# Kernel optimization log

Measured on AMD Instinct MI355X. Metric: run time of the kernel, lower is better.

The kernel has to match this reference:

```python
import jax, jax.numpy as jnp
import numpy as np

SEQ_LEN = 512
D_MODEL = 512
N_HEADS = 8
KERNEL = 7
E_DIM = D_MODEL // N_HEADS  # d_values = 64
PAD = KERNEL // 2


def _gen_D(L):
    D = np.zeros((L - 1, L), dtype=np.float32)
    D[:, 1:] += np.eye(L - 1, dtype=np.float32)
    D[:, :-1] -= np.eye(L - 1, dtype=np.float32)
    return D


def setup_inputs() -> dict:
    key = jax.random.key(0)
    k1, k2, k3 = jax.random.split(key, 3)
    B = 16
    values = jax.random.normal(k1, (B, SEQ_LEN, N_HEADS, E_DIM), dtype=jnp.float32)
    # second-order difference operator, then SVD of D^T D (as in __init__)
    D = _gen_D(SEQ_LEN - 1) @ _gen_D(SEQ_LEN)          # (L-2, L)
    U_np, S_np, _ = np.linalg.svd(D.T @ D)             # (L, L), (L,)
    U = jnp.asarray(U_np, dtype=jnp.float32)
    S = jnp.asarray(S_np, dtype=jnp.float32)
    # Conv1d(E, 1, kernel) parameters
    bound = 1.0 / np.sqrt(E_DIM * KERNEL)
    conv_w = jax.random.uniform(k2, (1, E_DIM, KERNEL), minval=-bound, maxval=bound, dtype=jnp.float32)
    conv_b = jax.random.uniform(k3, (1,), minval=-bound, maxval=bound, dtype=jnp.float32)
    return {"values": values, "conv_w": conv_w, "conv_b": conv_b, "U": U, "S": S}


def reference(values, conv_w, conv_b, U, S):
    B, L, H, E = values.shape
    # lambda predictor: conv1d over length with replicate padding, then 1+elu
    x = values.transpose(0, 2, 3, 1).reshape(B * H, E, L)          # (BH, E, L)
    xp = jnp.pad(x, ((0, 0), (0, 0), (PAD, PAD)), mode='edge')
    y = jax.lax.conv_general_dilated(
        xp, conv_w, window_strides=(1,), padding='VALID',
        dimension_numbers=('NCH', 'OIH', 'NCH'))                   # (BH, 1, L)
    y = y + conv_b[None, :, None]
    lambdas = 1.0 + jax.nn.elu(y).reshape(B, H, L).transpose(0, 2, 1)  # (B, L, H)
    # diagonal reweighting in the U basis: U diag(1/(1+lambda*S)) U^T @ values
    inv = 1.0 / (1.0 + jnp.einsum('blh,l->bhl', lambdas, S))       # (B, H, L)
    t = jnp.einsum('jm,bjhd->bhmd', U, values)                      # project onto U columns
    t = t * inv[..., None]                                          # diagonal scale (fused, no LxL diag)
    out = jnp.einsum('im,bhmd->bihd', U, t)                         # (B, L, H, E)
    return out
```

## Files before the change

### kernel.cpp

```cpp
#include <hip/hip_runtime.h>
#include <hip/hip_bf16.h>
#include <cstdint>
#include <cmath>

#define LSEQ 512
#define EDIM 64
#define NBIG 8192

typedef __attribute__((ext_vector_type(8))) short short8;
typedef __attribute__((ext_vector_type(8))) unsigned short ushort8v;
typedef __attribute__((ext_vector_type(4))) float f32x4;

__device__ __forceinline__ unsigned short f2bf(float f) {
    union { float f; unsigned int u; } x; x.f = f;
    unsigned int r = x.u + 0x7FFFu + ((x.u >> 16) & 1u);
    return (unsigned short)(r >> 16);
}

__device__ __forceinline__ void async_copy16(void* lds, const void* g) {
    auto g1 = (const __attribute__((address_space(1))) void*)g;
    auto l3 = (__attribute__((address_space(3))) void*)lds;
    __builtin_amdgcn_global_load_lds(g1, l3, 16, 0, 0);
}

__device__ __forceinline__ void store16_swz(unsigned short* rowptr, int cbase,
                                            int q, int row,
                                            const unsigned short* o) {
    int x = row & 7, x1 = x >> 1, x0 = x & 1;
    unsigned short* dst = rowptr + cbase + ((q ^ x1) << 4);
    ushort8v lo = *(const ushort8v*)o;
    ushort8v hi = *(const ushort8v*)(o + 8);
    if (x0) { *(ushort8v*)dst = hi; *(ushort8v*)(dst + 8) = lo; }
    else    { *(ushort8v*)dst = lo; *(ushort8v*)(dst + 8) = hi; }
}

__global__ __launch_bounds__(256) void prep_kernel(
        const float* __restrict__ vals, const float* __restrict__ U,
        const float* __restrict__ cw, const float* __restrict__ cb,
        const float* __restrict__ S,
        unsigned short* __restrict__ Vpp, unsigned short* __restrict__ Ut,
        unsigned short* __restrict__ Ub, float* __restrict__ inv) {
    __shared__ float Ls[70 * 65];
    __shared__ float red[16][64];
    __shared__ float wcoef[448];
    int id = blockIdx.x;
    int t = threadIdx.x;

    if (id < 1024) {
        int b = id >> 6, h = (id >> 3) & 7, jt = id & 7;
        int j0 = jt * 64;
        for (int idx = t; idx < 448; idx += 256) wcoef[idx] = cw[idx];
        const float* base = vals + (size_t)b * 262144 + h * 64;
        #pragma unroll
        for (int i = 0; i < 5; ++i) {
            int idx = i * 256 + t;
            if (idx < 1120) {
                int row = idx >> 4, c4 = (idx & 15) * 4;
                int grow = j0 + row - 3;
                grow = grow < 0 ? 0 : (grow > 511 ? 511 : grow);
                float4 v = *(const float4*)(base + (size_t)grow * 512 + c4);
                float* d = &Ls[row * 65 + c4];
                d[0] = v.x; d[1] = v.y; d[2] = v.z; d[3] = v.w;
            }
        }
        __syncthreads();

        {
            int e = t & 63, q = t >> 6;
            unsigned short o[16];
            #pragma unroll
            for (int jj = 0; jj < 16; ++jj)
                o[jj] = f2bf(Ls[(3 + q * 16 + jj) * 65 + e]);
            int n = b * 512 + h * 64 + e;
            store16_swz(Vpp + (size_t)n * 512, j0, q, n, o);
        }

        {
            int lg = t & 15, q16 = t >> 4;
            int l0 = lg * 4, e0 = q16 * 4;
            float rv[10][4];
            #pragma unroll
            for (int r = 0; r < 10; ++r)
                #pragma unroll
                for (int je = 0; je < 4; ++je)
                    rv[r][je] = Ls[(l0 + r) * 65 + e0 + je];
            float a4[4] = {0.f, 0.f, 0.f, 0.f};
            #pragma unroll
            for (int kk = 0; kk < 7; ++kk) {
                #pragma unroll
                for (int je = 0; je < 4; ++je) {
                    float w = wcoef[(e0 + je) * 7 + kk];
                    #pragma unroll
                    for (int dl = 0; dl < 4; ++dl)
                        a4[dl] += rv[dl + kk][je] * w;
                }
            }
            #pragma unroll
            for (int dl = 0; dl < 4; ++dl) red[q16][l0 + dl] = a4[dl];
        }
        __syncthreads();
        if (t < 64) {
            float y = cb[0];
            #pragma unroll
            for (int g = 0; g < 16; ++g) y += red[g][t];
            float lam = (y > 0.f) ? (1.f + y) : expf(y);
            inv[(size_t)(b * 8 + h) * 512 + j0 + t] = 1.f / (1.f + lam * S[j0 + t]);
        }
    } else {
        int id2 = id - 1024;
        int j0 = (id2 >> 3) * 64, m0 = (id2 & 7) * 64;
        int r = t >> 2, q = t & 3;
        int c16 = q * 16;
        float v[16];
        const float* src = U + (size_t)(j0 + r) * 512 + m0 + c16;
        #pragma unroll
        for (int k = 0; k < 16; k += 4) {
            float4 vv = *(const float4*)(src + k);
            v[k] = vv.x; v[k+1] = vv.y; v[k+2] = vv.z; v[k+3] = vv.w;
        }
        {
            unsigned short o[16];
            #pragma unroll
            for (int k = 0; k < 16; ++k) o[k] = f2bf(v[k]);
            store16_swz(Ub + (size_t)(j0 + r) * 512, m0, q, j0 + r, o);
        }
        #pragma unroll
        for (int k = 0; k < 16; ++k) Ls[r * 65 + c16 + k] = v[k];
        __syncthreads();
        {
            unsigned short o[16];
            #pragma unroll
            for (int k = 0; k < 16; ++k) o[k] = f2bf(Ls[(c16 + k) * 65 + r]);
            store16_swz(Ut + (size_t)(m0 + r) * 512, j0, q, m0 + r, o);
        }
    }
}

template<int EPI>
__launch_bounds__(256, 1)
__global__ void gemm_kernel(const unsigned short* __restrict__ A,
                            const unsigned short* __restrict__ B,
                            const float* __restrict__ inv,
                            unsigned short* __restrict__ Tout,
                            float* __restrict__ Out) {
    __shared__ __align__(16) unsigned short As[2][128 * 64];
    __shared__ __align__(16) unsigned short Bs[2][128 * 64];

    int bid = blockIdx.x;
    bid = (bid & 7) * 32 + (bid >> 3);
    int mt = bid & 3, nt = bid >> 2;
    int m0 = mt * 128, n0 = nt * 128;
    int t = threadIdx.x, lane = t & 63, wave = t >> 6;
    int wm = wave >> 1, wn = wave & 1;
    int l15 = lane & 15, l4 = lane >> 4;

    f32x4 acc[4][4] = {};

    const unsigned short* Ab = A + (size_t)(m0 + (t >> 3)) * 512 + (t & 7) * 8;
    const unsigned short* Bb = B + (size_t)(n0 + (t >> 3)) * 512 + (t & 7) * 8;

    auto STAGE = [&](int buf, int kk) {
        int ko = kk * 64;
        unsigned short* ap = &As[buf][t * 8];
        unsigned short* bp = &Bs[buf][t * 8];
        #pragma unroll
        for (int c = 0; c < 4; ++c) {
            async_copy16(ap + c * 2048, Ab + (size_t)(32 * c) * 512 + ko);
            async_copy16(bp + c * 2048, Bb + (size_t)(32 * c) * 512 + ko);
        }
    };
    auto COMPUTE = [&](int buf) {
        #pragma unroll
        for (int k2 = 0; k2 < 2; ++k2) {
            short8 a[4], bf[4];
            #pragma unroll
            for (int i = 0; i < 4; ++i) {
                int row = wm * 64 + i * 16 + l15;
                a[i] = *(const short8*)&As[buf][row * 64 + (((k2 * 4 + l4) ^ (row & 7)) << 3)];
            }
            #pragma unroll
            for (int j = 0; j < 4; ++j) {
                int row = wn * 64 + j * 16 + l15;
                bf[j] = *(const short8*)&Bs[buf][row * 64 + (((k2 * 4 + l4) ^ (row & 7)) << 3)];
            }
            #pragma unroll
            for (int i = 0; i < 4; ++i)
                #pragma unroll
                for (int j = 0; j < 4; ++j)
                    acc[i][j] = __builtin_amdgcn_mfma_f32_16x16x32_bf16(a[i], bf[j], acc[i][j], 0, 0, 0);
        }
    };

    STAGE(0, 0);
    __syncthreads();
    int cur = 0;
    #pragma unroll
    for (int kk = 0; kk < 7; ++kk) {
        STAGE(cur ^ 1, kk + 1);
        COMPUTE(cur);
        __syncthreads();
        cur ^= 1;
    }
    COMPUTE(cur);

    #pragma unroll
    for (int i = 0; i < 4; ++i) {
        int mb = m0 + wm * 64 + i * 16 + l4 * 4;
        if (EPI == 1) {
            int bh = nt * 2 + wn;
            float4 s = *(const float4*)&inv[(size_t)bh * 512 + mb];
            #pragma unroll
            for (int j = 0; j < 4; ++j) {
                int n = n0 + wn * 64 + j * 16 + l15;
                f32x4 v = acc[i][j];
                ushort4 pack;
                pack.x = f2bf(v[0] * s.x);
                pack.y = f2bf(v[1] * s.y);
                pack.z = f2bf(v[2] * s.z);
                pack.w = f2bf(v[3] * s.w);
                int e = mb & 63;
                int pos = (mb & ~63) + ((((e >> 3) ^ (n & 7)) << 3) | (e & 7));
                *(ushort4*)&Tout[(size_t)n * 512 + pos] = pack;
            }
        } else {
            #pragma unroll
            for (int j = 0; j < 4; ++j) {
                int n = n0 + wn * 64 + j * 16 + l15;
                int b = n >> 9, hd = n & 511;
                f32x4 v = acc[i][j];
                float* o = Out + (size_t)b * 262144 + (size_t)mb * 512 + hd;
                o[0] = v[0]; o[512] = v[1]; o[1024] = v[2]; o[1536] = v[3];
            }
        }
    }
}

extern "C" void kernel_launch(void* const* d_in, const int* in_sizes, int n_in,
                              void* d_out, int out_size, void* d_ws, size_t ws_size,
                              hipStream_t stream) {
    const float* vals = (const float*)d_in[0];
    const float* cw   = (const float*)d_in[1];
    const float* cb   = (const float*)d_in[2];
    const float* U    = (const float*)d_in[3];
    const float* S    = (const float*)d_in[4];
    float* out = (float*)d_out;

    const size_t off_Ut  = 0;
    const size_t off_Ub  = 524288;
    const size_t off_V   = 1048576;
    const size_t off_T   = 9437184;
    const size_t off_inv = 17825792;
    const size_t ws_need = 18087936;
    if (ws_size < ws_need) return;

    char* ws = (char*)d_ws;
    unsigned short* Ut  = (unsigned short*)(ws + off_Ut);
    unsigned short* Ub  = (unsigned short*)(ws + off_Ub);
    unsigned short* Vpp = (unsigned short*)(ws + off_V);
    unsigned short* Tpp = (unsigned short*)(ws + off_T);
    float*          inv = (float*)(ws + off_inv);

    prep_kernel<<<1088, 256, 0, stream>>>(vals, U, cw, cb, S, Vpp, Ut, Ub, inv);
    gemm_kernel<1><<<256, 256, 0, stream>>>(Ut, Vpp, inv, Tpp, nullptr);
    gemm_kernel<2><<<256, 256, 0, stream>>>(Ub, Tpp, nullptr, nullptr, out);
}
```

Before: 37.36 us.

## Split GEMM K-loop across two wave groups with LDS reduction

Doubles the GEMM block size to 512 threads. The two halves of the block each handle one 32-wide K half of every 64-wide tile and are combined through a shared-memory reduction before the epilogue. The aim is more waves per CU for latency hiding, since only 256 blocks run with occupancy 1. The cost is an extra LDS write and read pass plus barriers, and half the waves sit idle during the epilogue.

```diff
diff --git a/kernel.cpp b/kernel.cpp
--- a/kernel.cpp
+++ b/kernel.cpp
@@ -137,7 +137,7 @@
 }
 
 template<int EPI>
-__launch_bounds__(256, 1)
+__launch_bounds__(512, 1)
 __global__ void gemm_kernel(const unsigned short* __restrict__ A,
                             const unsigned short* __restrict__ B,
                             const float* __restrict__ inv,
@@ -151,7 +151,7 @@
     int mt = bid & 3, nt = bid >> 2;
     int m0 = mt * 128, n0 = nt * 128;
     int t = threadIdx.x, lane = t & 63, wave = t >> 6;
-    int wm = wave >> 1, wn = wave & 1;
+    int kh = wave >> 2, wm = (wave >> 1) & 1, wn = wave & 1;
     int l15 = lane & 15, l4 = lane >> 4;
 
     f32x4 acc[4][4] = {};
@@ -163,32 +163,28 @@
         int ko = kk * 64;
         unsigned short* ap = &As[buf][t * 8];
         unsigned short* bp = &Bs[buf][t * 8];
-        #pragma unroll
-        for (int c = 0; c < 4; ++c) {
-            async_copy16(ap + c * 2048, Ab + (size_t)(32 * c) * 512 + ko);
-            async_copy16(bp + c * 2048, Bb + (size_t)(32 * c) * 512 + ko);
-        }
+        async_copy16(ap,        Ab + ko);
+        async_copy16(ap + 4096, Ab + (size_t)64 * 512 + ko);
+        async_copy16(bp,        Bb + ko);
+        async_copy16(bp + 4096, Bb + (size_t)64 * 512 + ko);
     };
     auto COMPUTE = [&](int buf) {
-        #pragma unroll
-        for (int k2 = 0; k2 < 2; ++k2) {
-            short8 a[4], bf[4];
-            #pragma unroll
-            for (int i = 0; i < 4; ++i) {
-                int row = wm * 64 + i * 16 + l15;
-                a[i] = *(const short8*)&As[buf][row * 64 + (((k2 * 4 + l4) ^ (row & 7)) << 3)];
-            }
-            #pragma unroll
-            for (int j = 0; j < 4; ++j) {
-                int row = wn * 64 + j * 16 + l15;
-                bf[j] = *(const short8*)&Bs[buf][row * 64 + (((k2 * 4 + l4) ^ (row & 7)) << 3)];
-            }
-            #pragma unroll
-            for (int i = 0; i < 4; ++i)
-                #pragma unroll
-                for (int j = 0; j < 4; ++j)
-                    acc[i][j] = __builtin_amdgcn_mfma_f32_16x16x32_bf16(a[i], bf[j], acc[i][j], 0, 0, 0);
-        }
+        short8 a[4], bf[4];
+        #pragma unroll
+        for (int i = 0; i < 4; ++i) {
+            int row = wm * 64 + i * 16 + l15;
+            a[i] = *(const short8*)&As[buf][row * 64 + (((kh * 4 + l4) ^ (row & 7)) << 3)];
+        }
+        #pragma unroll
+        for (int j = 0; j < 4; ++j) {
+            int row = wn * 64 + j * 16 + l15;
+            bf[j] = *(const short8*)&Bs[buf][row * 64 + (((kh * 4 + l4) ^ (row & 7)) << 3)];
+        }
+        #pragma unroll
+        for (int i = 0; i < 4; ++i)
+            #pragma unroll
+            for (int j = 0; j < 4; ++j)
+                acc[i][j] = __builtin_amdgcn_mfma_f32_16x16x32_bf16(a[i], bf[j], acc[i][j], 0, 0, 0);
     };
 
     STAGE(0, 0);
@@ -202,17 +198,42 @@
         cur ^= 1;
     }
     COMPUTE(cur);
+    __syncthreads();
+
+    int q = wm * 2 + wn;
+    float* red = (q < 2 ? (float*)As : (float*)Bs) + (q & 1) * 4096;
+    if (kh == 1) {
+        #pragma unroll
+        for (int i = 0; i < 4; ++i)
+            #pragma unroll
+            for (int j = 0; j < 4; ++j) {
+                int mloc = i * 16 + l4 * 4, nloc = j * 16 + l15;
+                f32x4 v = acc[i][j];
+                red[(mloc + 0) * 64 + nloc] = v[0];
+                red[(mloc + 1) * 64 + nloc] = v[1];
+                red[(mloc + 2) * 64 + nloc] = v[2];
+                red[(mloc + 3) * 64 + nloc] = v[3];
+            }
+    }
+    __syncthreads();
+    if (kh == 1) return;
 
     #pragma unroll
     for (int i = 0; i < 4; ++i) {
         int mb = m0 + wm * 64 + i * 16 + l4 * 4;
+        int mloc = i * 16 + l4 * 4;
         if (EPI == 1) {
             int bh = nt * 2 + wn;
             float4 s = *(const float4*)&inv[(size_t)bh * 512 + mb];
             #pragma unroll
             for (int j = 0; j < 4; ++j) {
                 int n = n0 + wn * 64 + j * 16 + l15;
+                int nloc = j * 16 + l15;
                 f32x4 v = acc[i][j];
+                v[0] += red[(mloc + 0) * 64 + nloc];
+                v[1] += red[(mloc + 1) * 64 + nloc];
+                v[2] += red[(mloc + 2) * 64 + nloc];
+                v[3] += red[(mloc + 3) * 64 + nloc];
                 ushort4 pack;
                 pack.x = f2bf(v[0] * s.x);
                 pack.y = f2bf(v[1] * s.y);
@@ -226,8 +247,13 @@
             #pragma unroll
             for (int j = 0; j < 4; ++j) {
                 int n = n0 + wn * 64 + j * 16 + l15;
+                int nloc = j * 16 + l15;
                 int b = n >> 9, hd = n & 511;
                 f32x4 v = acc[i][j];
+                v[0] += red[(mloc + 0) * 64 + nloc];
+                v[1] += red[(mloc + 1) * 64 + nloc];
+                v[2] += red[(mloc + 2) * 64 + nloc];
+                v[3] += red[(mloc + 3) * 64 + nloc];
                 float* o = Out + (size_t)b * 262144 + (size_t)mb * 512 + hd;
                 o[0] = v[0]; o[512] = v[1]; o[1024] = v[2]; o[1536] = v[3];
             }
@@ -261,6 +287,6 @@
     float*          inv = (float*)(ws + off_inv);
 
     prep_kernel<<<1088, 256, 0, stream>>>(vals, U, cw, cb, S, Vpp, Ut, Ub, inv);
-    gemm_kernel<1><<<256, 256, 0, stream>>>(Ut, Vpp, inv, Tpp, nullptr);
-    gemm_kernel<2><<<256, 256, 0, stream>>>(Ub, Tpp, nullptr, nullptr, out);
-}
+    gemm_kernel<1><<<256, 512, 0, stream>>>(Ut, Vpp, inv, Tpp, nullptr);
+    gemm_kernel<2><<<256, 512, 0, stream>>>(Ub, Tpp, nullptr, nullptr, out);
+}
```

After: 37.69 us. No clear change (+0.9%).
